# Optimization experiments

Hardware: AMD Instinct MI355X
Metric: run time of the kernel (lower is better)

## Reference

```python
import jax, jax.numpy as jnp
import numpy as np

B = 4096      # batch
D_IN = 512    # input_dim
D = 256       # d_model
T = 424       # n_targets
L = 6         # num_layers
EPS = 1e-5    # torch LayerNorm default


def _ln(x, g, b):
    m = jnp.mean(x, axis=-1, keepdims=True)
    v = jnp.var(x, axis=-1, keepdims=True)
    return (x - m) * jax.lax.rsqrt(v + EPS) * g + b


def setup_inputs() -> dict:
    key = jax.random.key(0)
    ks = iter(jax.random.split(key, 32))
    r = lambda shape, s=0.05: jax.random.normal(next(ks), shape, dtype=jnp.float32) * s
    return {
        'x': jax.random.normal(next(ks), (B, D_IN), dtype=jnp.float32),
        'proj_W': r((4, D // 4, D_IN)), 'proj_b': r((4, D // 4)),
        'attn_in_W': r((L, 3 * D, D)), 'attn_in_b': r((L, 3 * D)),
        'attn_out_W': r((L, D, D)), 'attn_out_b': r((L, D)),
        'ln_g': jnp.ones((L, D), jnp.float32), 'ln_b': jnp.zeros((L, D), jnp.float32),
        'ff_W1': r((L, 4 * D, D)), 'ff_b1': r((L, 4 * D)),
        'ff_W2': r((L, D, 4 * D)), 'ff_b2': r((L, D)),
        'cross_in_W': r((3 * D, D)), 'cross_in_b': r((3 * D,)),
        'cross_out_W': r((D, D)), 'cross_out_b': r((D,)),
        'tp_W1': r((T, D // 2, D)), 'tp_b1': r((T, D // 2)),
        'tp_ln_g': jnp.ones((T, D // 2), jnp.float32), 'tp_ln_b': jnp.zeros((T, D // 2), jnp.float32),
        'tp_W2': r((T, D // 4, D // 2)), 'tp_b2': r((T, D // 4)),
        'tp_W3': r((T, D // 4)), 'tp_b3': r((T,)),
    }


def reference(x, proj_W, proj_b, attn_in_W, attn_in_b, attn_out_W, attn_out_b,
              ln_g, ln_b, ff_W1, ff_b1, ff_W2, ff_b2,
              cross_in_W, cross_in_b, cross_out_W, cross_out_b,
              tp_W1, tp_b1, tp_ln_g, tp_ln_b, tp_W2, tp_b2, tp_W3, tp_b3):
    # 4 feature projections -> concat == reshape of stacked einsum  [B, 4, D/4] -> [B, D]
    h = jnp.einsum('bd,pkd->bpk', x, proj_W) + proj_b
    h = h.reshape(h.shape[0], D)

    # 6 transformer blocks on seq_len=1: softmax over a single key == 1, so
    # MHA(x,x,x) reduces exactly to out_proj(v_proj(x)); dropout = identity (eval).
    for i in range(L):
        Wv, bv = attn_in_W[i, 2 * D:], attn_in_b[i, 2 * D:]
        attn = (h @ Wv.T + bv) @ attn_out_W[i].T + attn_out_b[i]
        h = _ln(h + attn, ln_g[i], ln_b[i])          # same norm instance reused
        ff = jax.nn.gelu(h @ ff_W1[i].T + ff_b1[i], approximate=False) @ ff_W2[i].T + ff_b2[i]
        h = _ln(h + ff, ln_g[i], ln_b[i])

    # cross-target attention, also seq_len=1 -> v/out projections only
    Wv, bv = cross_in_W[2 * D:], cross_in_b[2 * D:]
    h = h + ((h @ Wv.T + bv) @ cross_out_W.T + cross_out_b)

    # 424 per-target MLP heads, batched as grouped GEMMs
    t = jnp.einsum('bd,tkd->btk', h, tp_W1) + tp_b1          # [B, T, 128]
    t = jax.nn.relu(_ln(t, tp_ln_g, tp_ln_b))
    t = jax.nn.relu(jnp.einsum('btk,tmk->btm', t, tp_W2) + tp_b2)  # [B, T, 64]
    out = jnp.einsum('btm,tm->bt', t, tp_W3) + tp_b3         # [B, T]
    return out
```

## Files before the change

### kernel.cpp

```cpp
#include <hip/hip_runtime.h>
#include <stdint.h>

using bf16x8 = __attribute__((ext_vector_type(8))) short;
using f32x4  = __attribute__((ext_vector_type(4))) float;

__device__ __forceinline__ f32x4 mfma16(bf16x8 a, bf16x8 b, f32x4 c) {
  return __builtin_amdgcn_mfma_f32_16x16x32_bf16(a, b, c, 0, 0, 0);
}

__device__ __forceinline__ unsigned short f2b_rne(float f) {
  union { float f; unsigned u; } v; v.f = f;
  unsigned r = v.u + 0x7fffu + ((v.u >> 16) & 1u);
  return (unsigned short)(r >> 16);
}

__global__ void f2b_kernel(const float* __restrict__ s, unsigned short* __restrict__ d, int n4) {
  int i = blockIdx.x * 256 + threadIdx.x;
  if (i >= n4) return;
  float4 v = reinterpret_cast<const float4*>(s)[i];
  ushort4 o;
  o.x = f2b_rne(v.x); o.y = f2b_rne(v.y); o.z = f2b_rne(v.z); o.w = f2b_rne(v.w);
  reinterpret_cast<ushort4*>(d)[i] = o;
}

__global__ __launch_bounds__(256) void compose_attn(
    const float* __restrict__ aiW, const float* __restrict__ aib,
    const float* __restrict__ aoW, const float* __restrict__ aob,
    const float* __restrict__ ciW, const float* __restrict__ cib,
    const float* __restrict__ coW, const float* __restrict__ cob,
    unsigned short* __restrict__ wEff, float* __restrict__ bEff) {
  const int mat = blockIdx.y;
  const float* Wo = (mat < 6) ? aoW + (size_t)mat * 65536 : coW;
  const float* Wv = (mat < 6) ? aiW + (size_t)mat * 196608 + 131072 : ciW + 131072;
  const float* bv = (mat < 6) ? aib + mat * 768 + 512 : cib + 512;
  const float* bo = (mat < 6) ? aob + mat * 256 : cob;
  unsigned short* Wd = wEff + (size_t)mat * 65536;
  const int m = blockIdx.x * 16 + (threadIdx.x >> 4);
  const int k0 = (threadIdx.x & 15) * 16;
  float c[16] = {};
  for (int j = 0; j < 256; ++j) {
    const float a = Wo[m * 256 + j];
    const float* Br = Wv + j * 256 + k0;
#pragma unroll
    for (int kk = 0; kk < 16; ++kk) c[kk] = fmaf(a, Br[kk], c[kk]);
  }
#pragma unroll
  for (int kk = 0; kk < 16; ++kk) Wd[m * 256 + k0 + kk] = f2b_rne(c[kk]);
  if (blockIdx.x == 0) {
    const int mm = threadIdx.x;
    float s = 0.f;
    for (int j = 0; j < 256; ++j) s = fmaf(Wo[mm * 256 + j], bv[j], s);
    bEff[mat * 256 + mm] = s + bo[mm];
  }
}

template<int EPI, int ROWS, int K>
__global__ __launch_bounds__(256, 4) void gemm_t2(
    const unsigned short* __restrict__ A, const unsigned short* __restrict__ W,
    const float* __restrict__ bias, float* __restrict__ hf,
    unsigned short* __restrict__ ybf, const float* __restrict__ gam,
    const float* __restrict__ bet, int Nout) {
  constexpr int NBF = ROWS / 16;
  constexpr int NCF = (ROWS == 16) ? 4 : 2;
  constexpr int NK = K / 32;
  constexpr int K2 = K * 2;
  __shared__ char smA[ROWS * K2];
  __shared__ float red[2][4][16];
  const int tid = threadIdx.x, wid = tid >> 6, lane = tid & 63;
  const int r = lane & 15, hi = lane >> 4;
  const int row0 = blockIdx.x * ROWS;
  const int colW0 = ((ROWS == 16) ? 0 : blockIdx.y * 128) + wid * (NCF * 16);

  constexpr int CHUNKS = ROWS * K / 8;
  constexpr int CPR = K / 8;
#pragma unroll
  for (int id = tid; id < CHUNKS; id += 256) {
    const int row = id / CPR, c8 = id % CPR;
    bf16x8 v = *reinterpret_cast<const bf16x8*>(A + (size_t)(row0 + row) * K + c8 * 8);
    *reinterpret_cast<bf16x8*>(smA + row * K2 + ((c8 * 16) ^ ((row & 7) << 4))) = v;
  }
  __syncthreads();

  const unsigned short* Wb = W + (size_t)(colW0 + r) * K + hi * 8;
  f32x4 acc[NBF][NCF] = {};
  bf16x8 wc[NCF], wn[NCF];
#pragma unroll
  for (int cf = 0; cf < NCF; ++cf)
    wc[cf] = *reinterpret_cast<const bf16x8*>(Wb + cf * 16 * K);
#pragma unroll 4
  for (int ks = 0; ks < NK; ++ks) {
    if (ks + 1 < NK) {
#pragma unroll
      for (int cf = 0; cf < NCF; ++cf)
        wn[cf] = *reinterpret_cast<const bf16x8*>(Wb + cf * 16 * K + (ks + 1) * 32);
    }
    bf16x8 av[NBF];
#pragma unroll
    for (int bf = 0; bf < NBF; ++bf)
      av[bf] = *reinterpret_cast<const bf16x8*>(
          smA + (bf * 16 + r) * K2 + ((ks * 64 + hi * 16) ^ ((r & 7) << 4)));
#pragma unroll
    for (int bf = 0; bf < NBF; ++bf)
#pragma unroll
      for (int cf = 0; cf < NCF; ++cf)
        acc[bf][cf] = mfma16(av[bf], wc[cf], acc[bf][cf]);
#pragma unroll
    for (int cf = 0; cf < NCF; ++cf) wc[cf] = wn[cf];
  }

  if (EPI == 1) {
#pragma unroll
    for (int bf = 0; bf < NBF; ++bf)
#pragma unroll
      for (int cf = 0; cf < NCF; ++cf) {
        const int col = colW0 + cf * 16 + r;
        const float bv = bias[col];
#pragma unroll
        for (int j = 0; j < 4; ++j) {
          const int row = row0 + bf * 16 + hi * 4 + j;
          float y = acc[bf][cf][j] + bv;
          y = 0.5f * y * (1.f + erff(y * 0.70710678118654752f));
          ybf[(size_t)row * Nout + col] = f2b_rne(y);
        }
      }
  } else if (EPI == 2 || EPI == 4) {
#pragma unroll
    for (int bf = 0; bf < NBF; ++bf)
#pragma unroll
      for (int cf = 0; cf < NCF; ++cf) {
        const int col = colW0 + cf * 16 + r;
        const float bv = bias[col];
#pragma unroll
        for (int j = 0; j < 4; ++j) {
          const int row = row0 + bf * 16 + hi * 4 + j;
          float y = acc[bf][cf][j] + bv;
          if (EPI == 4) y += hf[(size_t)row * 256 + col];
          hf[(size_t)row * 256 + col]  = y;
          ybf[(size_t)row * 256 + col] = f2b_rne(y);
        }
      }
  } else {
    float xx[4][4];
    float sum[4] = {0.f, 0.f, 0.f, 0.f}, sq[4] = {0.f, 0.f, 0.f, 0.f};
#pragma unroll
    for (int cf = 0; cf < 4; ++cf) {
      const int col = colW0 + cf * 16 + r;
      const float bv = bias[col];
#pragma unroll
      for (int j = 0; j < 4; ++j) {
        float v = hf[(size_t)(row0 + hi * 4 + j) * 256 + col] + acc[0][cf][j] + bv;
        xx[cf][j] = v; sum[j] += v; sq[j] += v * v;
      }
    }
#pragma unroll
    for (int m = 1; m < 16; m <<= 1) {
#pragma unroll
      for (int j = 0; j < 4; ++j) {
        sum[j] += __shfl_xor(sum[j], m, 64);
        sq[j]  += __shfl_xor(sq[j],  m, 64);
      }
    }
    if (r == 0) {
#pragma unroll
      for (int j = 0; j < 4; ++j) { red[0][wid][hi * 4 + j] = sum[j]; red[1][wid][hi * 4 + j] = sq[j]; }
    }
    __syncthreads();
    float mu[4], rs[4];
#pragma unroll
    for (int j = 0; j < 4; ++j) {
      const int rr = hi * 4 + j;
      float ts = red[0][0][rr] + red[0][1][rr] + red[0][2][rr] + red[0][3][rr];
      float tq = red[1][0][rr] + red[1][1][rr] + red[1][2][rr] + red[1][3][rr];
      float mean = ts * (1.f / 256.f);
      mu[j] = mean;
      rs[j] = rsqrtf(tq * (1.f / 256.f) - mean * mean + 1e-5f);
    }
#pragma unroll
    for (int cf = 0; cf < 4; ++cf) {
      const int col = colW0 + cf * 16 + r;
      const float gm = gam[col], bb = bet[col];
#pragma unroll
      for (int j = 0; j < 4; ++j) {
        const int row = row0 + hi * 4 + j;
        float y = (xx[cf][j] - mu[j]) * rs[j] * gm + bb;
        hf[(size_t)row * 256 + col]  = y;
        ybf[(size_t)row * 256 + col] = f2b_rne(y);
      }
    }
  }
}

__global__ __launch_bounds__(512, 2) void phase_d2(
    const unsigned short* __restrict__ hbf, const unsigned short* __restrict__ w1b,
    const float* __restrict__ b1, const float* __restrict__ lng, const float* __restrict__ lnb,
    const unsigned short* __restrict__ w2b, const float* __restrict__ b2,
    const float* __restrict__ w3, const float* __restrict__ b3,
    float* __restrict__ out) {
  __shared__ char sm[149504];
  const int tid = threadIdx.x, wid = tid >> 6, lane = tid & 63;
  const int r = lane & 15, hi = lane >> 4;
  const int sw = (r & 7) << 4;
  const int t = blockIdx.y;

  const unsigned short* w1t = w1b + (size_t)t * 32768;
  const unsigned short* w2t = w2b + (size_t)t * 8192;
#pragma unroll
  for (int i = 0; i < 8; ++i) {
    const int id = tid + i * 512;
    const int c = id >> 5, s = id & 31;
    bf16x8 v = *reinterpret_cast<const bf16x8*>(w1t + c * 256 + s * 8);
    *reinterpret_cast<bf16x8*>(sm + c * 512 + ((s * 16) ^ ((c & 7) << 4))) = v;
  }
#pragma unroll
  for (int i = 0; i < 2; ++i) {
    const int id = tid + i * 512;
    const int c = id >> 4, s = id & 15;
    bf16x8 v = *reinterpret_cast<const bf16x8*>(w2t + c * 128 + s * 8);
    *reinterpret_cast<bf16x8*>(sm + 65536 + c * 256 + ((s * 16) ^ ((c & 7) << 4))) = v;
  }
  {
    float v;
    if (tid < 128)      v = b1 [t * 128 + tid];
    else if (tid < 256) v = lng[t * 128 + tid - 128];
    else if (tid < 384) v = lnb[t * 128 + tid - 256];
    else if (tid < 448) v = b2 [t * 64  + tid - 384];
    else                v = w3 [t * 64  + tid - 448];
    reinterpret_cast<float*>(sm + 81920)[tid] = v;
  }
  __syncthreads();

  const float* cb1 = reinterpret_cast<const float*>(sm + 81920);
  const float* cg  = cb1 + 128;
  const float* cbe = cb1 + 256;
  const float* cb2 = cb1 + 384;
  const float* cw3 = cb1 + 448;
  char* t1w = sm + 83968 + wid * 8192;
  const float b3t = b3[t];
  const int token_b0 = blockIdx.x * 1024;

  for (int tile = 0; tile < 2; ++tile) {
    const int B0 = token_b0 + tile * 512 + wid * 64;

    f32x4 acc1[8][4] = {};
    bf16x8 bc[4], bn[4];
#pragma unroll
    for (int bf = 0; bf < 4; ++bf)
      bc[bf] = *reinterpret_cast<const bf16x8*>(hbf + (size_t)(B0 + bf * 16 + r) * 256 + hi * 8);
#pragma unroll
    for (int ks = 0; ks < 8; ++ks) {
      bf16x8 a[8];
#pragma unroll
      for (int cf = 0; cf < 8; ++cf)
        a[cf] = *reinterpret_cast<const bf16x8*>(sm + (cf * 16 + r) * 512 + ((ks * 64 + hi * 16) ^ sw));
      if (ks < 7) {
#pragma unroll
        for (int bf = 0; bf < 4; ++bf)
          bn[bf] = *reinterpret_cast<const bf16x8*>(hbf + (size_t)(B0 + bf * 16 + r) * 256 + (ks + 1) * 32 + hi * 8);
      }
      __builtin_amdgcn_s_setprio(1);
#pragma unroll
      for (int cf = 0; cf < 8; ++cf)
#pragma unroll
        for (int bf = 0; bf < 4; ++bf)
          acc1[cf][bf] = mfma16(a[cf], bc[bf], acc1[cf][bf]);
      __builtin_amdgcn_s_setprio(0);
#pragma unroll
      for (int bf = 0; bf < 4; ++bf) bc[bf] = bn[bf];
    }

#pragma unroll
    for (int cf = 0; cf < 8; ++cf) {
      f32x4 b1v = *reinterpret_cast<const f32x4*>(cb1 + cf * 16 + hi * 4);
#pragma unroll
      for (int bf = 0; bf < 4; ++bf) acc1[cf][bf] += b1v;
    }

    float mu[4], rsd[4];
#pragma unroll
    for (int bf = 0; bf < 4; ++bf) {
      float s = 0.f, s2 = 0.f;
#pragma unroll
      for (int cf = 0; cf < 8; ++cf)
#pragma unroll
        for (int j = 0; j < 4; ++j) { float v = acc1[cf][bf][j]; s += v; s2 += v * v; }
      s  += __shfl_xor(s, 16, 64);  s  += __shfl_xor(s, 32, 64);
      s2 += __shfl_xor(s2, 16, 64); s2 += __shfl_xor(s2, 32, 64);
      const float m = s * (1.f / 128.f);
      mu[bf] = m;
      rsd[bf] = rsqrtf(s2 * (1.f / 128.f) - m * m + 1e-5f);
    }

    f32x4 acc2[4][4] = {};
#pragma unroll
    for (int half = 0; half < 2; ++half) {
#pragma unroll
      for (int cf = 0; cf < 8; ++cf) {
        f32x4 gv = *reinterpret_cast<const f32x4*>(cg  + cf * 16 + hi * 4);
        f32x4 bv = *reinterpret_cast<const f32x4*>(cbe + cf * 16 + hi * 4);
#pragma unroll
        for (int bl = 0; bl < 2; ++bl) {
          const int bf = half * 2 + bl;
          unsigned o01, o23;
          {
            float y0 = fmaxf((acc1[cf][bf][0] - mu[bf]) * rsd[bf] * gv[0] + bv[0], 0.f);
            float y1 = fmaxf((acc1[cf][bf][1] - mu[bf]) * rsd[bf] * gv[1] + bv[1], 0.f);
            float y2 = fmaxf((acc1[cf][bf][2] - mu[bf]) * rsd[bf] * gv[2] + bv[2], 0.f);
            float y3 = fmaxf((acc1[cf][bf][3] - mu[bf]) * rsd[bf] * gv[3] + bv[3], 0.f);
            o01 = (unsigned)f2b_rne(y0) | ((unsigned)f2b_rne(y1) << 16);
            o23 = (unsigned)f2b_rne(y2) | ((unsigned)f2b_rne(y3) << 16);
          }
          uint2 pk; pk.x = o01; pk.y = o23;
          *reinterpret_cast<uint2*>(t1w + (bl * 16 + r) * 256 + ((cf * 32 + hi * 8) ^ sw)) = pk;
        }
      }
#pragma unroll
      for (int ks = 0; ks < 4; ++ks) {
        bf16x8 a2[4];
#pragma unroll
        for (int cf2 = 0; cf2 < 4; ++cf2)
          a2[cf2] = *reinterpret_cast<const bf16x8*>(sm + 65536 + (cf2 * 16 + r) * 256 + ((ks * 64 + hi * 16) ^ sw));
        __builtin_amdgcn_s_setprio(1);
#pragma unroll
        for (int bl = 0; bl < 2; ++bl) {
          bf16x8 bb = *reinterpret_cast<const bf16x8*>(t1w + (bl * 16 + r) * 256 + ((ks * 64 + hi * 16) ^ sw));
#pragma unroll
          for (int cf2 = 0; cf2 < 4; ++cf2)
            acc2[cf2][half * 2 + bl] = mfma16(a2[cf2], bb, acc2[cf2][half * 2 + bl]);
        }
        __builtin_amdgcn_s_setprio(0);
      }
    }

    float s[4] = {0.f, 0.f, 0.f, 0.f};
#pragma unroll
    for (int cf2 = 0; cf2 < 4; ++cf2) {
      f32x4 b2v = *reinterpret_cast<const f32x4*>(cb2 + cf2 * 16 + hi * 4);
      f32x4 w3v = *reinterpret_cast<const f32x4*>(cw3 + cf2 * 16 + hi * 4);
#pragma unroll
      for (int bf = 0; bf < 4; ++bf)
#pragma unroll
        for (int j = 0; j < 4; ++j)
          s[bf] += fmaxf(acc2[cf2][bf][j] + b2v[j], 0.f) * w3v[j];
    }
#pragma unroll
    for (int bf = 0; bf < 4; ++bf) {
      s[bf] += __shfl_xor(s[bf], 16, 64);
      s[bf] += __shfl_xor(s[bf], 32, 64);
      if (hi == 0) out[(size_t)(B0 + bf * 16 + r) * 424 + t] = s[bf] + b3t;
    }
  }
}

extern "C" void kernel_launch(void* const* d_in, const int* in_sizes, int n_in,
                              void* d_out, int out_size, void* d_ws, size_t ws_size,
                              hipStream_t stream) {
  const float* x     = (const float*)d_in[0];
  const float* projW = (const float*)d_in[1];
  const float* projb = (const float*)d_in[2];
  const float* aiW   = (const float*)d_in[3];
  const float* aib   = (const float*)d_in[4];
  const float* aoW   = (const float*)d_in[5];
  const float* aob   = (const float*)d_in[6];
  const float* lng   = (const float*)d_in[7];
  const float* lnbp  = (const float*)d_in[8];
  const float* f1W   = (const float*)d_in[9];
  const float* f1b   = (const float*)d_in[10];
  const float* f2W   = (const float*)d_in[11];
  const float* f2bp  = (const float*)d_in[12];
  const float* ciW   = (const float*)d_in[13];
  const float* cib   = (const float*)d_in[14];
  const float* coW   = (const float*)d_in[15];
  const float* cob   = (const float*)d_in[16];
  const float* tpW1  = (const float*)d_in[17];
  const float* tpb1  = (const float*)d_in[18];
  const float* tplng = (const float*)d_in[19];
  const float* tplnb = (const float*)d_in[20];
  const float* tpW2  = (const float*)d_in[21];
  const float* tpb2  = (const float*)d_in[22];
  const float* tpW3  = (const float*)d_in[23];
  const float* tpb3  = (const float*)d_in[24];
  float* out = (float*)d_out;

  char* ws = (char*)d_ws;
  size_t off = 0;
  auto alloc = [&](size_t n) { char* p = ws + off; off = (off + n + 255) & ~(size_t)255; return p; };
  unsigned short* xb   = (unsigned short*)alloc(4096ull * 512 * 2);
  unsigned short* pWb  = (unsigned short*)alloc(256ull * 512 * 2);
  unsigned short* f1Wb = (unsigned short*)alloc(6ull * 1024 * 256 * 2);
  unsigned short* f2Wb = (unsigned short*)alloc(6ull * 256 * 1024 * 2);
  unsigned short* W1b  = (unsigned short*)alloc(424ull * 128 * 256 * 2);
  unsigned short* W2b  = (unsigned short*)alloc(424ull * 64 * 128 * 2);
  unsigned short* wEff = (unsigned short*)alloc(7ull * 256 * 256 * 2);
  float*          bEff = (float*)alloc(7ull * 256 * 4);
  float*          hf   = (float*)alloc(4096ull * 256 * 4);
  unsigned short* hbf  = (unsigned short*)alloc(4096ull * 256 * 2);
  unsigned short* gbf  = (unsigned short*)alloc(4096ull * 1024 * 2);

  auto conv = [&](const float* s, unsigned short* d, size_t n) {
    int n4 = (int)(n >> 2);
    f2b_kernel<<<dim3((n4 + 255) / 256), dim3(256), 0, stream>>>(s, d, n4);
  };
  compose_attn<<<dim3(16, 7), dim3(256), 0, stream>>>(aiW, aib, aoW, aob, ciW, cib, coW, cob, wEff, bEff);
  conv(x, xb, 4096ull * 512);
  conv(projW, pWb, 256ull * 512);
  conv(f1W, f1Wb, 6ull * 1024 * 256);
  conv(f2W, f2Wb, 6ull * 256 * 1024);
  conv(tpW1, W1b, 424ull * 128 * 256);
  conv(tpW2, W2b, 424ull * 64 * 128);

  dim3 blk(256);
  gemm_t2<2, 32, 512><<<dim3(128, 2), blk, 0, stream>>>(xb, pWb, projb, hf, hbf, nullptr, nullptr, 256);
  for (int i = 0; i < 6; ++i) {
    gemm_t2<3, 16, 256><<<dim3(256, 1), blk, 0, stream>>>(hbf, wEff + (size_t)i * 65536, bEff + i * 256,
                                                          hf, hbf, lng + i * 256, lnbp + i * 256, 256);
    gemm_t2<1, 32, 256><<<dim3(128, 8), blk, 0, stream>>>(hbf, f1Wb + (size_t)i * 1024 * 256, f1b + i * 1024,
                                                          nullptr, gbf, nullptr, nullptr, 1024);
    gemm_t2<3, 16, 1024><<<dim3(256, 1), blk, 0, stream>>>(gbf, f2Wb + (size_t)i * 256 * 1024, f2bp + i * 256,
                                                           hf, hbf, lng + i * 256, lnbp + i * 256, 256);
  }
  gemm_t2<4, 32, 256><<<dim3(128, 2), blk, 0, stream>>>(hbf, wEff + 6ull * 65536, bEff + 6 * 256,
                                                        hf, hbf, nullptr, nullptr, 256);

  phase_d2<<<dim3(4, 424), dim3(512), 0, stream>>>(hbf, W1b, tpb1, tplng, tplnb, W2b, tpb2, tpW3, tpb3, out);
}
```

Baseline: 621.8 us.

## Fuse entire transformer trunk into one persistent per-row-tile kernel

Replaces the 20 separate GEMM launches for the projection, six transformer layers and cross-attention with a single kernel. Each 512-thread block owns 16 rows, keeps the hidden state in registers and the bf16 activations and GELU output in shared memory, and streams weights from global/L2 with a 3-deep register prefetch. This removes launch overhead and the global round-trips of hf/hbf/gbf between layers. The cost is that only 256 blocks run, and every block rereads all the trunk weights. Separately, the s_setprio hints in the head kernel are removed.

```diff
diff --git a/kernel.cpp b/kernel.cpp
--- a/kernel.cpp
+++ b/kernel.cpp
@@ -54,140 +54,176 @@
   }
 }
 
-template<int EPI, int ROWS, int K>
-__global__ __launch_bounds__(256, 4) void gemm_t2(
-    const unsigned short* __restrict__ A, const unsigned short* __restrict__ W,
-    const float* __restrict__ bias, float* __restrict__ hf,
-    unsigned short* __restrict__ ybf, const float* __restrict__ gam,
-    const float* __restrict__ bet, int Nout) {
-  constexpr int NBF = ROWS / 16;
-  constexpr int NCF = (ROWS == 16) ? 4 : 2;
-  constexpr int NK = K / 32;
-  constexpr int K2 = K * 2;
-  __shared__ char smA[ROWS * K2];
-  __shared__ float red[2][4][16];
+template<int NCF, int K, int NK>
+__device__ __forceinline__ void gemm_ws(const unsigned short* __restrict__ Wb,
+                                        const char* __restrict__ smA_r,
+                                        int hi16, int swz, f32x4 (&acc)[NCF]) {
+  bf16x8 w[3][NCF];
+#pragma unroll
+  for (int p = 0; p < 2; ++p)
+#pragma unroll
+    for (int cf = 0; cf < NCF; ++cf)
+      w[p][cf] = *reinterpret_cast<const bf16x8*>(Wb + (size_t)cf * 16 * K + p * 32);
+#pragma unroll
+  for (int ks = 0; ks < NK; ++ks) {
+    const bf16x8 a = *reinterpret_cast<const bf16x8*>(smA_r + ((ks * 64 + hi16) ^ swz));
+    if (ks + 2 < NK) {
+#pragma unroll
+      for (int cf = 0; cf < NCF; ++cf)
+        w[(ks + 2) % 3][cf] = *reinterpret_cast<const bf16x8*>(Wb + (size_t)cf * 16 * K + (ks + 2) * 32);
+    }
+#pragma unroll
+    for (int cf = 0; cf < NCF; ++cf)
+      acc[cf] = mfma16(a, w[ks % 3][cf], acc[cf]);
+  }
+}
+
+__global__ __launch_bounds__(512, 2) void trunk_fused(
+    const unsigned short* __restrict__ xb, const unsigned short* __restrict__ pWb,
+    const float* __restrict__ projb,
+    const unsigned short* __restrict__ wEff, const float* __restrict__ bEff,
+    const unsigned short* __restrict__ f1Wb, const float* __restrict__ f1b,
+    const unsigned short* __restrict__ f2Wb, const float* __restrict__ f2bp,
+    const float* __restrict__ lng, const float* __restrict__ lnb,
+    unsigned short* __restrict__ hbf) {
+  __shared__ char hbuf[16 * 512];
+  __shared__ char gbuf[16 * 2048];
+  __shared__ float red[2][16][8];
   const int tid = threadIdx.x, wid = tid >> 6, lane = tid & 63;
   const int r = lane & 15, hi = lane >> 4;
-  const int row0 = blockIdx.x * ROWS;
-  const int colW0 = ((ROWS == 16) ? 0 : blockIdx.y * 128) + wid * (NCF * 16);
-
-  constexpr int CHUNKS = ROWS * K / 8;
-  constexpr int CPR = K / 8;
-#pragma unroll
-  for (int id = tid; id < CHUNKS; id += 256) {
-    const int row = id / CPR, c8 = id % CPR;
-    bf16x8 v = *reinterpret_cast<const bf16x8*>(A + (size_t)(row0 + row) * K + c8 * 8);
-    *reinterpret_cast<bf16x8*>(smA + row * K2 + ((c8 * 16) ^ ((row & 7) << 4))) = v;
+  const int swz = (r & 7) << 4, hi16 = hi * 16;
+  const int row0 = blockIdx.x << 4;
+  const int colb = wid * 32;
+
+#pragma unroll
+  for (int i = 0; i < 2; ++i) {
+    const int id = tid + i * 512, row = id >> 6, c8 = id & 63;
+    bf16x8 v = *reinterpret_cast<const bf16x8*>(xb + (size_t)(row0 + row) * 512 + c8 * 8);
+    *reinterpret_cast<bf16x8*>(gbuf + row * 1024 + ((c8 * 16) ^ ((row & 7) << 4))) = v;
   }
   __syncthreads();
 
-  const unsigned short* Wb = W + (size_t)(colW0 + r) * K + hi * 8;
-  f32x4 acc[NBF][NCF] = {};
-  bf16x8 wc[NCF], wn[NCF];
-#pragma unroll
-  for (int cf = 0; cf < NCF; ++cf)
-    wc[cf] = *reinterpret_cast<const bf16x8*>(Wb + cf * 16 * K);
-#pragma unroll 4
-  for (int ks = 0; ks < NK; ++ks) {
-    if (ks + 1 < NK) {
-#pragma unroll
-      for (int cf = 0; cf < NCF; ++cf)
-        wn[cf] = *reinterpret_cast<const bf16x8*>(Wb + cf * 16 * K + (ks + 1) * 32);
-    }
-    bf16x8 av[NBF];
-#pragma unroll
-    for (int bf = 0; bf < NBF; ++bf)
-      av[bf] = *reinterpret_cast<const bf16x8*>(
-          smA + (bf * 16 + r) * K2 + ((ks * 64 + hi * 16) ^ ((r & 7) << 4)));
-#pragma unroll
-    for (int bf = 0; bf < NBF; ++bf)
-#pragma unroll
-      for (int cf = 0; cf < NCF; ++cf)
-        acc[bf][cf] = mfma16(av[bf], wc[cf], acc[bf][cf]);
-#pragma unroll
-    for (int cf = 0; cf < NCF; ++cf) wc[cf] = wn[cf];
-  }
-
-  if (EPI == 1) {
-#pragma unroll
-    for (int bf = 0; bf < NBF; ++bf)
-#pragma unroll
-      for (int cf = 0; cf < NCF; ++cf) {
-        const int col = colW0 + cf * 16 + r;
-        const float bv = bias[col];
-#pragma unroll
-        for (int j = 0; j < 4; ++j) {
-          const int row = row0 + bf * 16 + hi * 4 + j;
-          float y = acc[bf][cf][j] + bv;
-          y = 0.5f * y * (1.f + erff(y * 0.70710678118654752f));
-          ybf[(size_t)row * Nout + col] = f2b_rne(y);
-        }
-      }
-  } else if (EPI == 2 || EPI == 4) {
-#pragma unroll
-    for (int bf = 0; bf < NBF; ++bf)
-#pragma unroll
-      for (int cf = 0; cf < NCF; ++cf) {
-        const int col = colW0 + cf * 16 + r;
-        const float bv = bias[col];
-#pragma unroll
-        for (int j = 0; j < 4; ++j) {
-          const int row = row0 + bf * 16 + hi * 4 + j;
-          float y = acc[bf][cf][j] + bv;
-          if (EPI == 4) y += hf[(size_t)row * 256 + col];
-          hf[(size_t)row * 256 + col]  = y;
-          ybf[(size_t)row * 256 + col] = f2b_rne(y);
-        }
-      }
-  } else {
-    float xx[4][4];
-    float sum[4] = {0.f, 0.f, 0.f, 0.f}, sq[4] = {0.f, 0.f, 0.f, 0.f};
-#pragma unroll
-    for (int cf = 0; cf < 4; ++cf) {
-      const int col = colW0 + cf * 16 + r;
-      const float bv = bias[col];
+  f32x4 hreg[2];
+
+  auto store_hb = [&]() {
+#pragma unroll
+    for (int cf = 0; cf < 2; ++cf) {
+      const int cb = (colb + cf * 16 + r) * 2;
 #pragma unroll
       for (int j = 0; j < 4; ++j) {
-        float v = hf[(size_t)(row0 + hi * 4 + j) * 256 + col] + acc[0][cf][j] + bv;
-        xx[cf][j] = v; sum[j] += v; sq[j] += v * v;
-      }
-    }
-#pragma unroll
-    for (int m = 1; m < 16; m <<= 1) {
+        const int row = hi * 4 + j;
+        *reinterpret_cast<unsigned short*>(hbuf + row * 512 + (cb ^ ((row & 7) << 4))) =
+            f2b_rne(hreg[cf][j]);
+      }
+    }
+  };
+
+  auto ln_apply = [&](float gm0, float gm1, float bb0, float bb1) {
+    float sum[4], sq[4];
+#pragma unroll
+    for (int j = 0; j < 4; ++j) {
+      const float v0 = hreg[0][j], v1 = hreg[1][j];
+      sum[j] = v0 + v1; sq[j] = v0 * v0 + v1 * v1;
+    }
+#pragma unroll
+    for (int m = 1; m < 16; m <<= 1)
 #pragma unroll
       for (int j = 0; j < 4; ++j) {
         sum[j] += __shfl_xor(sum[j], m, 64);
         sq[j]  += __shfl_xor(sq[j],  m, 64);
       }
-    }
-    if (r == 0) {
-#pragma unroll
-      for (int j = 0; j < 4; ++j) { red[0][wid][hi * 4 + j] = sum[j]; red[1][wid][hi * 4 + j] = sq[j]; }
-    }
+    if (r == 0)
+#pragma unroll
+      for (int j = 0; j < 4; ++j) {
+        red[0][hi * 4 + j][wid] = sum[j];
+        red[1][hi * 4 + j][wid] = sq[j];
+      }
     __syncthreads();
-    float mu[4], rs[4];
 #pragma unroll
     for (int j = 0; j < 4; ++j) {
-      const int rr = hi * 4 + j;
-      float ts = red[0][0][rr] + red[0][1][rr] + red[0][2][rr] + red[0][3][rr];
-      float tq = red[1][0][rr] + red[1][1][rr] + red[1][2][rr] + red[1][3][rr];
-      float mean = ts * (1.f / 256.f);
-      mu[j] = mean;
-      rs[j] = rsqrtf(tq * (1.f / 256.f) - mean * mean + 1e-5f);
-    }
-#pragma unroll
-    for (int cf = 0; cf < 4; ++cf) {
-      const int col = colW0 + cf * 16 + r;
-      const float gm = gam[col], bb = bet[col];
-#pragma unroll
-      for (int j = 0; j < 4; ++j) {
-        const int row = row0 + hi * 4 + j;
-        float y = (xx[cf][j] - mu[j]) * rs[j] * gm + bb;
-        hf[(size_t)row * 256 + col]  = y;
-        ybf[(size_t)row * 256 + col] = f2b_rne(y);
-      }
-    }
-  }
+      const int row = hi * 4 + j;
+      f32x4 p0 = *reinterpret_cast<const f32x4*>(&red[0][row][0]);
+      f32x4 p1 = *reinterpret_cast<const f32x4*>(&red[0][row][4]);
+      f32x4 q0 = *reinterpret_cast<const f32x4*>(&red[1][row][0]);
+      f32x4 q1 = *reinterpret_cast<const f32x4*>(&red[1][row][4]);
+      const float ts = p0[0]+p0[1]+p0[2]+p0[3]+p1[0]+p1[1]+p1[2]+p1[3];
+      const float tq = q0[0]+q0[1]+q0[2]+q0[3]+q1[0]+q1[1]+q1[2]+q1[3];
+      const float mean = ts * (1.f / 256.f);
+      const float rstd = rsqrtf(tq * (1.f / 256.f) - mean * mean + 1e-5f);
+      hreg[0][j] = (hreg[0][j] - mean) * rstd * gm0 + bb0;
+      hreg[1][j] = (hreg[1][j] - mean) * rstd * gm1 + bb1;
+    }
+  };
+
+  {
+    f32x4 acc[2] = {};
+    gemm_ws<2, 512, 16>(pWb + (size_t)(colb + r) * 512 + hi * 8, gbuf + r * 1024, hi16, swz, acc);
+    const float bv0 = projb[colb + r], bv1 = projb[colb + 16 + r];
+#pragma unroll
+    for (int j = 0; j < 4; ++j) { hreg[0][j] = acc[0][j] + bv0; hreg[1][j] = acc[1][j] + bv1; }
+  }
+  store_hb();
+  __syncthreads();
+
+  for (int L = 0; L < 6; ++L) {
+    const float gm0 = lng[L * 256 + colb + r],      gm1 = lng[L * 256 + colb + 16 + r];
+    const float bb0 = lnb[L * 256 + colb + r],      bb1 = lnb[L * 256 + colb + 16 + r];
+    {
+      f32x4 acc[2] = {};
+      gemm_ws<2, 256, 8>(wEff + (size_t)L * 65536 + (size_t)(colb + r) * 256 + hi * 8,
+                         hbuf + r * 512, hi16, swz, acc);
+      const float be0 = bEff[L * 256 + colb + r], be1 = bEff[L * 256 + colb + 16 + r];
+#pragma unroll
+      for (int j = 0; j < 4; ++j) { hreg[0][j] += acc[0][j] + be0; hreg[1][j] += acc[1][j] + be1; }
+    }
+    ln_apply(gm0, gm1, bb0, bb1);
+    store_hb();
+    __syncthreads();
+    {
+      f32x4 accf[8] = {};
+      gemm_ws<8, 256, 8>(f1Wb + (size_t)L * 262144 + (size_t)(wid * 128 + r) * 256 + hi * 8,
+                         hbuf + r * 512, hi16, swz, accf);
+#pragma unroll
+      for (int cf = 0; cf < 8; ++cf) {
+        const int colw = wid * 128 + cf * 16 + r;
+        const float bv = f1b[L * 1024 + colw];
+        const int cb = colw * 2;
+#pragma unroll
+        for (int j = 0; j < 4; ++j) {
+          float y = accf[cf][j] + bv;
+          y = 0.5f * y * (1.f + erff(y * 0.70710678118654752f));
+          const int row = hi * 4 + j;
+          *reinterpret_cast<unsigned short*>(gbuf + row * 2048 + (cb ^ ((row & 7) << 4))) = f2b_rne(y);
+        }
+      }
+    }
+    __syncthreads();
+    {
+      f32x4 acc[2] = {};
+      gemm_ws<2, 1024, 32>(f2Wb + (size_t)L * 262144 + (size_t)(colb + r) * 1024 + hi * 8,
+                           gbuf + r * 2048, hi16, swz, acc);
+      const float be0 = f2bp[L * 256 + colb + r], be1 = f2bp[L * 256 + colb + 16 + r];
+#pragma unroll
+      for (int j = 0; j < 4; ++j) { hreg[0][j] += acc[0][j] + be0; hreg[1][j] += acc[1][j] + be1; }
+    }
+    ln_apply(gm0, gm1, bb0, bb1);
+    store_hb();
+    __syncthreads();
+  }
+
+  {
+    f32x4 acc[2] = {};
+    gemm_ws<2, 256, 8>(wEff + 6ull * 65536 + (size_t)(colb + r) * 256 + hi * 8,
+                       hbuf + r * 512, hi16, swz, acc);
+    const float be0 = bEff[1536 + colb + r], be1 = bEff[1536 + colb + 16 + r];
+#pragma unroll
+    for (int j = 0; j < 4; ++j) { hreg[0][j] += acc[0][j] + be0; hreg[1][j] += acc[1][j] + be1; }
+  }
+#pragma unroll
+  for (int cf = 0; cf < 2; ++cf)
+#pragma unroll
+    for (int j = 0; j < 4; ++j)
+      hbf[(size_t)(row0 + hi * 4 + j) * 256 + colb + cf * 16 + r] = f2b_rne(hreg[cf][j]);
 }
 
 __global__ __launch_bounds__(512, 2) void phase_d2(
@@ -257,13 +293,11 @@
         for (int bf = 0; bf < 4; ++bf)
           bn[bf] = *reinterpret_cast<const bf16x8*>(hbf + (size_t)(B0 + bf * 16 + r) * 256 + (ks + 1) * 32 + hi * 8);
       }
-      __builtin_amdgcn_s_setprio(1);
 #pragma unroll
       for (int cf = 0; cf < 8; ++cf)
 #pragma unroll
         for (int bf = 0; bf < 4; ++bf)
           acc1[cf][bf] = mfma16(a[cf], bc[bf], acc1[cf][bf]);
-      __builtin_amdgcn_s_setprio(0);
 #pragma unroll
       for (int bf = 0; bf < 4; ++bf) bc[bf] = bn[bf];
     }
@@ -319,7 +353,6 @@
 #pragma unroll
         for (int cf2 = 0; cf2 < 4; ++cf2)
           a2[cf2] = *reinterpret_cast<const bf16x8*>(sm + 65536 + (cf2 * 16 + r) * 256 + ((ks * 64 + hi * 16) ^ sw));
-        __builtin_amdgcn_s_setprio(1);
 #pragma unroll
         for (int bl = 0; bl < 2; ++bl) {
           bf16x8 bb = *reinterpret_cast<const bf16x8*>(t1w + (bl * 16 + r) * 256 + ((ks * 64 + hi * 16) ^ sw));
@@ -327,7 +360,6 @@
           for (int cf2 = 0; cf2 < 4; ++cf2)
             acc2[cf2][half * 2 + bl] = mfma16(a2[cf2], bb, acc2[cf2][half * 2 + bl]);
         }
-        __builtin_amdgcn_s_setprio(0);
       }
     }
 
@@ -392,9 +424,7 @@
   unsigned short* W2b  = (unsigned short*)alloc(424ull * 64 * 128 * 2);
   unsigned short* wEff = (unsigned short*)alloc(7ull * 256 * 256 * 2);
   float*          bEff = (float*)alloc(7ull * 256 * 4);
-  float*          hf   = (float*)alloc(4096ull * 256 * 4);
   unsigned short* hbf  = (unsigned short*)alloc(4096ull * 256 * 2);
-  unsigned short* gbf  = (unsigned short*)alloc(4096ull * 1024 * 2);
 
   auto conv = [&](const float* s, unsigned short* d, size_t n) {
     int n4 = (int)(n >> 2);
@@ -408,18 +438,8 @@
   conv(tpW1, W1b, 424ull * 128 * 256);
   conv(tpW2, W2b, 424ull * 64 * 128);
 
-  dim3 blk(256);
-  gemm_t2<2, 32, 512><<<dim3(128, 2), blk, 0, stream>>>(xb, pWb, projb, hf, hbf, nullptr, nullptr, 256);
-  for (int i = 0; i < 6; ++i) {
-    gemm_t2<3, 16, 256><<<dim3(256, 1), blk, 0, stream>>>(hbf, wEff + (size_t)i * 65536, bEff + i * 256,
-                                                          hf, hbf, lng + i * 256, lnbp + i * 256, 256);
-    gemm_t2<1, 32, 256><<<dim3(128, 8), blk, 0, stream>>>(hbf, f1Wb + (size_t)i * 1024 * 256, f1b + i * 1024,
-                                                          nullptr, gbf, nullptr, nullptr, 1024);
-    gemm_t2<3, 16, 1024><<<dim3(256, 1), blk, 0, stream>>>(gbf, f2Wb + (size_t)i * 256 * 1024, f2bp + i * 256,
-                                                           hf, hbf, lng + i * 256, lnbp + i * 256, 256);
-  }
-  gemm_t2<4, 32, 256><<<dim3(128, 2), blk, 0, stream>>>(hbf, wEff + 6ull * 65536, bEff + 6 * 256,
-                                                        hf, hbf, nullptr, nullptr, 256);
+  trunk_fused<<<dim3(256), dim3(512), 0, stream>>>(
+      xb, pWb, projb, wEff, bEff, f1Wb, f1b, f2Wb, f2bp, lng, lnbp, hbf);
 
   phase_d2<<<dim3(4, 424), dim3(512), 0, stream>>>(hbf, W1b, tpb1, tplng, tplnb, W2b, tpb2, tpW3, tpb3, out);
 }
```

Result: faster. 559.1 us (-10.1%).
